# Kernel tuning notes

Measured on AMD Instinct MI355X. Metric: run time of the kernel, lower is better.

The kernel has to match this reference:

```python
import jax, jax.numpy as jnp
import numpy as np

B, L, D, T = 32, 1024, 1024, 10  # batch, seq_len, d_model, num_tags


def setup_inputs() -> dict:
    key = jax.random.key(0)
    ks = jax.random.split(key, 6)
    embeddings = jax.random.normal(ks[0], (B, L, D), jnp.float32)
    attention_mask = jnp.ones((B, L), jnp.int32)  # torchcrf requires mask[:,0]==1
    labels = jax.random.randint(ks[1], (B, L), 0, T)
    conv_w = jax.random.normal(ks[2], (T, D, 3), jnp.float32) * 0.02  # [out,in,k] torch layout
    conv_b = jnp.zeros((T,), jnp.float32)
    start_transitions = jax.random.uniform(ks[3], (T,), jnp.float32, -0.1, 0.1)
    end_transitions = jax.random.uniform(ks[4], (T,), jnp.float32, -0.1, 0.1)
    transitions = jax.random.uniform(ks[5], (T, T), jnp.float32, -0.1, 0.1)
    return dict(embeddings=embeddings, attention_mask=attention_mask, labels=labels,
                conv_w=conv_w, conv_b=conv_b, start_transitions=start_transitions,
                end_transitions=end_transitions, transitions=transitions)


def _crf_nll(emissions, labels, mask_bool, start_transitions, end_transitions, transitions):
    # emissions [B,L,T], labels [B,L] int, mask_bool [B,L]
    b, l, t = emissions.shape
    maskf = mask_bool.astype(emissions.dtype)
    # ---- numerator: score of the given tag path ----
    em_tag = jnp.take_along_axis(emissions, labels[..., None], axis=-1)[..., 0]  # [B,L]
    trans_sc = transitions[labels[:, :-1], labels[:, 1:]]                         # [B,L-1]
    num = start_transitions[labels[:, 0]] + em_tag[:, 0]
    num = num + ((trans_sc + em_tag[:, 1:]) * maskf[:, 1:]).sum(-1)
    seq_len = maskf.sum(-1).astype(jnp.int32)                                     # [B]
    last_tags = labels[jnp.arange(b), seq_len - 1]
    num = num + end_transitions[last_tags]
    # ---- denominator: forward algorithm (log partition), lax.scan over time ----
    alpha0 = start_transitions + emissions[:, 0]                                  # [B,T]

    def step(alpha, xs):
        em_t, m_t = xs  # [B,T], [B]
        nxt = jax.nn.logsumexp(alpha[:, :, None] + transitions[None] + em_t[:, None, :], axis=1)
        return jnp.where(m_t[:, None], nxt, alpha), None

    alpha, _ = jax.lax.scan(step, alpha0,
                            (emissions[:, 1:].transpose(1, 0, 2), mask_bool[:, 1:].T))
    denom = jax.nn.logsumexp(alpha + end_transitions, axis=1)                     # [B]
    return -(num - denom).sum()  # torchcrf reduction='sum', model negates


def reference(embeddings, attention_mask, labels, conv_w, conv_b,
              start_transitions, end_transitions, transitions):
    # Conv1d(d_model -> num_tags, k=3, padding='same') on [B,D,L]
    x = embeddings.transpose(0, 2, 1)  # [B,D,L]
    em = jax.lax.conv_general_dilated(x, conv_w, (1,), 'SAME',
                                      dimension_numbers=('NCH', 'OIH', 'NCH'))
    em = em.transpose(0, 2, 1) + conv_b  # [B,L,T]
    mask_bool = attention_mask.astype(bool)
    return _crf_nll(em, labels, mask_bool, start_transitions, end_transitions, transitions)
```

## Files before the change

kernel.cpp:

```cpp
#include <hip/hip_runtime.h>


#define LNEG -1e30f

static constexpr int B = 32, L = 1024, D = 1024;
static constexpr int CS = 64;
static constexpr int NC = 16;

static constexpr size_t EMPAD_OFF    = 0;
static constexpr size_t CHUNKP_OFF   = (size_t)B * L * 16;
static constexpr size_t CHUNKOFF_OFF = CHUNKP_OFF + (size_t)B * NC * 100;
static constexpr size_t WB_OFF       = CHUNKOFF_OFF + (size_t)B * NC * 12;

typedef __attribute__((ext_vector_type(8))) short short8;
typedef __attribute__((ext_vector_type(4))) short short4v;
typedef __attribute__((ext_vector_type(4))) float v4f;

static __device__ inline short f2bf(float f) {
    unsigned u = __float_as_uint(f);
    unsigned r = (u + 0x7FFFu + ((u >> 16) & 1u)) >> 16;
    return (short)r;
}

__global__ __launch_bounds__(256) void init_kernel(
    const float* __restrict__ w, const float* __restrict__ bias,
    float* __restrict__ emPad, short* __restrict__ WB, float* __restrict__ out)
{
    const int gid    = blockIdx.x * 256 + threadIdx.x;
    const int stride = gridDim.x * 256;

    for (int i = gid; i < B * L * 16; i += stride) {
        const int t = i & 15;
        emPad[i] = (t < 10) ? bias[t] : LNEG;
    }
    for (int i = gid; i < 49152; i += stride) {
        const int k8 = i >> 7;
        const int r  = i & 127;
        const int t  = r >> 3;
        const int j  = r & 7;
        const int k  = (k8 << 3) | j;
        const int kk = k >> 10;
        const int d  = k & 1023;
        WB[i] = (t < 10) ? f2bf(w[t * (D * 3) + d * 3 + kk]) : (short)0;
    }
    if (gid == 0) out[0] = 0.f;
}

static constexpr int SROW = 136;
static constexpr int LDSN = 18 * SROW;

__global__ __launch_bounds__(64) void conv_mfma_kernel(
    const float* __restrict__ emb, const short* __restrict__ WB,
    float* __restrict__ emPad)
{
    __shared__ short lds[2 * LDSN];

    const int lane = threadIdx.x;
    const unsigned bid = blockIdx.x;
    const int dh   = bid & 1;
    const int l0   = ((bid >> 1) & 63) << 4;
    const int b    = bid >> 7;
    const int g    = lane >> 4;
    const int m    = lane & 15;

    const float* embB = emb + (size_t)b * (L * D);

    v4f acc0 = {0.f, 0.f, 0.f, 0.f};
    v4f acc1 = {0.f, 0.f, 0.f, 0.f};
    v4f acc2 = {0.f, 0.f, 0.f, 0.f};

    float4 pre[9];

#define PREF(DC) do {                                                         \
    const int d0_ = (DC) * 128;                                               \
    _Pragma("unroll")                                                         \
    for (int it = 0; it < 9; ++it) {                                          \
        const int idx = lane + it * 64;                                       \
        const int r_ = idx >> 5, c4 = idx & 31;                               \
        const int gl = l0 + r_ - 1;                                           \
        float4 v = make_float4(0.f, 0.f, 0.f, 0.f);                           \
        if ((unsigned)gl < (unsigned)L)                                       \
            v = *(const float4*)(embB + (size_t)gl * D + d0_ + c4 * 4);       \
        pre[it] = v;                                                          \
    } } while (0)

#define COMMIT(BUF) do {                                                      \
    short* base_ = lds + (BUF) * LDSN;                                        \
    _Pragma("unroll")                                                         \
    for (int it = 0; it < 9; ++it) {                                          \
        const int idx = lane + it * 64;                                       \
        const int r_ = idx >> 5, c4 = idx & 31;                               \
        short4v s;                                                            \
        s.x = f2bf(pre[it].x); s.y = f2bf(pre[it].y);                         \
        s.z = f2bf(pre[it].z); s.w = f2bf(pre[it].w);                         \
        *(short4v*)(base_ + r_ * SROW + c4 * 4) = s;                          \
    } } while (0)

    const int dcBase = dh * 4;
    PREF(dcBase);
    COMMIT(0);
    __syncthreads();

    for (int q = 0; q < 4; ++q) {
        const int dc = dcBase + q;
        if (q < 3) PREF(dc + 1);

        const short* bufp = lds + (q & 1) * LDSN;
#pragma unroll
        for (int kk = 0; kk < 3; ++kk) {
            const short* arow = bufp + (m + kk) * SROW + g * 8;
            const short* wp   = WB + ((size_t)(kk * 128 + dc * 16 + g)) * 128 + m * 8;
#pragma unroll
            for (int ds = 0; ds < 4; ++ds) {
                const short8 a  = *(const short8*)(arow + ds * 32);
                const short8 bf = *(const short8*)(wp + (size_t)ds * 4 * 128);
                if (kk == 0)      acc0 = __builtin_amdgcn_mfma_f32_16x16x32_bf16(a, bf, acc0, 0, 0, 0);
                else if (kk == 1) acc1 = __builtin_amdgcn_mfma_f32_16x16x32_bf16(a, bf, acc1, 0, 0, 0);
                else              acc2 = __builtin_amdgcn_mfma_f32_16x16x32_bf16(a, bf, acc2, 0, 0, 0);
            }
        }

        if (q < 3) COMMIT((q + 1) & 1);
        __syncthreads();
    }
#undef PREF
#undef COMMIT

    if (m < 10) {
#pragma unroll
        for (int r = 0; r < 4; ++r) {
            const int row = g * 4 + r;
            const int pos = l0 + row;
            atomicAdd(&emPad[((size_t)(b * L + pos) << 4) + m],
                      acc0[r] + acc1[r] + acc2[r]);
        }
    }
}

__global__ __launch_bounds__(64) void crf_chunk_kernel(
    const float* __restrict__ emPad, const float* __restrict__ trans,
    const float* __restrict__ startT, const float* __restrict__ endT,
    const int* __restrict__ labels,
    float* __restrict__ chunkP, float* __restrict__ chunkOff,
    float* __restrict__ out)
{
    const int lane = threadIdx.x & 63;
    const int grp  = lane >> 4;
    const int i    = lane & 15;
    const int id   = blockIdx.x * 4 + grp;
    const int b    = id >> 4;
    const int c    = id & 15;

    float E[10][10];
#pragma unroll
    for (int k = 0; k < 10; ++k)
#pragma unroll
        for (int j = 0; j < 10; ++j)
            E[k][j] = __expf(trans[k * 10 + j]);

    float P[10];
#pragma unroll
    for (int j = 0; j < 10; ++j) P[j] = (i == j) ? 1.f : 0.f;
    float off = 0.f;

    const int l0 = 1 + c * CS;
    const int n  = min(CS, L - l0);
    const float* embp = emPad + ((size_t)(b * L + l0) << 4);

    float4 nx0 = *(const float4*)(embp);
    float4 nx1 = *(const float4*)(embp + 4);
    float2 nx2 = *(const float2*)(embp + 8);

    for (int s = 0; s < n; ++s) {
        const float4 e0 = nx0;
        const float4 e1 = nx1;
        const float2 e2 = nx2;
        if (s + 1 < n) {
            const float* p = embp + ((size_t)(s + 1) << 4);
            nx0 = *(const float4*)(p);
            nx1 = *(const float4*)(p + 4);
            nx2 = *(const float2*)(p + 8);
        }
        float sj[10];
        sj[0] = __expf(e0.x); sj[1] = __expf(e0.y); sj[2] = __expf(e0.z); sj[3] = __expf(e0.w);
        sj[4] = __expf(e1.x); sj[5] = __expf(e1.y); sj[6] = __expf(e1.z); sj[7] = __expf(e1.w);
        sj[8] = __expf(e2.x); sj[9] = __expf(e2.y);

        float C[10];
#pragma unroll
        for (int j = 0; j < 10; ++j) C[j] = P[0] * E[0][j];
#pragma unroll
        for (int k = 1; k < 10; ++k)
#pragma unroll
            for (int j = 0; j < 10; ++j)
                C[j] = fmaf(P[k], E[k][j], C[j]);
#pragma unroll
        for (int j = 0; j < 10; ++j) C[j] *= sj[j];

        float r = C[0];
#pragma unroll
        for (int j = 1; j < 10; ++j) r = fmaxf(r, C[j]);
        r = fmaxf(r, 1e-30f);
        const float inv = 1.f / r;
        off += __logf(r);
#pragma unroll
        for (int j = 0; j < 10; ++j) P[j] = C[j] * inv;
    }

    if (i < 10) {
        float* op = chunkP + (size_t)id * 100 + i * 10;
#pragma unroll
        for (int j = 0; j < 10; ++j) op[j] = P[j];
        chunkOff[id * 12 + i] = off;
    }

    const int* lab = labels + b * L;
    float part = 0.f;
#pragma unroll
    for (int q = 0; q < 4; ++q) {
        const int o = q * 16 + i;
        if (o < n) {
            const int pos = l0 + o;
            const int y  = lab[pos];
            const int yp = lab[pos - 1];
            part += emPad[((size_t)(b * L + pos) << 4) + y] + trans[yp * 10 + y];
            if (pos == L - 1) part += endT[y];
        }
    }
    if (c == 0 && i == 0) {
        const int y0 = lab[0];
        part += startT[y0] + emPad[((size_t)(b * L) << 4) + y0];
    }
#pragma unroll
    for (int sft = 8; sft >= 1; sft >>= 1) part += __shfl_xor(part, sft);
    if (i == 0) atomicAdd(out, -part);
}

__global__ __launch_bounds__(64) void crf_final_kernel(
    const float* __restrict__ emPad, const float* __restrict__ chunkP,
    const float* __restrict__ chunkOff, const float* __restrict__ startT,
    const float* __restrict__ endT, float* __restrict__ out)
{
    const int b = threadIdx.x;
    if (b >= B) return;

    float PA[10];
    float offA;
    {
        const float* e0 = emPad + ((size_t)(b * L) << 4);
        float A[10];
#pragma unroll
        for (int j = 0; j < 10; ++j) A[j] = startT[j] + e0[j];
        float m0 = A[0];
#pragma unroll
        for (int j = 1; j < 10; ++j) m0 = fmaxf(m0, A[j]);
#pragma unroll
        for (int j = 0; j < 10; ++j) PA[j] = __expf(A[j] - m0);
        offA = m0;
    }

    for (int c = 0; c < NC; ++c) {
        const int id = b * NC + c;
        const float* mp = chunkP + (size_t)id * 100;
        const float* op = chunkOff + id * 12;

        float mat[100];
#pragma unroll
        for (int q = 0; q < 25; ++q)
            *(float4*)&mat[q * 4] = *(const float4*)(mp + q * 4);
        float off[10];
#pragma unroll
        for (int k = 0; k < 10; ++k) off[k] = op[k];

        float mB = off[0];
#pragma unroll
        for (int k = 1; k < 10; ++k) mB = fmaxf(mB, off[k]);
        float gk[10];
#pragma unroll
        for (int k = 0; k < 10; ++k) gk[k] = PA[k] * __expf(off[k] - mB);

        float C[10];
#pragma unroll
        for (int j = 0; j < 10; ++j) C[j] = gk[0] * mat[j];
#pragma unroll
        for (int k = 1; k < 10; ++k)
#pragma unroll
            for (int j = 0; j < 10; ++j)
                C[j] = fmaf(gk[k], mat[k * 10 + j], C[j]);

        float r = C[0];
#pragma unroll
        for (int j = 1; j < 10; ++j) r = fmaxf(r, C[j]);
        r = fmaxf(r, 1e-30f);
        const float inv = 1.f / r;
        offA += mB + __logf(r);
#pragma unroll
        for (int j = 0; j < 10; ++j) PA[j] = C[j] * inv;
    }

    float s = 0.f;
#pragma unroll
    for (int j = 0; j < 10; ++j) s += PA[j] * __expf(endT[j]);
    atomicAdd(out, offA + __logf(s));
}

extern "C" void kernel_launch(void* const* d_in, const int* in_sizes, int n_in,
                              void* d_out, int out_size, void* d_ws, size_t ws_size,
                              hipStream_t stream)
{
    const float* emb    = (const float*)d_in[0];
    const int*   labels = (const int*)d_in[2];
    const float* conv_w = (const float*)d_in[3];
    const float* conv_b = (const float*)d_in[4];
    const float* startT = (const float*)d_in[5];
    const float* endT   = (const float*)d_in[6];
    const float* trans  = (const float*)d_in[7];

    float* ws       = (float*)d_ws;
    float* emPad    = ws + EMPAD_OFF;
    float* chunkP   = ws + CHUNKP_OFF;
    float* chunkOff = ws + CHUNKOFF_OFF;
    short* WB       = (short*)(ws + WB_OFF);
    float* outp     = (float*)d_out;

    hipLaunchKernelGGL(init_kernel, dim3(256), dim3(256), 0, stream,
                       conv_w, conv_b, emPad, WB, outp);
    hipLaunchKernelGGL(conv_mfma_kernel, dim3(B * 64 * 2), dim3(64), 0, stream,
                       emb, WB, emPad);
    hipLaunchKernelGGL(crf_chunk_kernel, dim3(B * NC / 4), dim3(64), 0, stream,
                       emPad, trans, startT, endT, labels, chunkP, chunkOff, outp);
    hipLaunchKernelGGL(crf_final_kernel, dim3(1), dim3(64), 0, stream,
                       emPad, chunkP, chunkOff, startT, endT, outp);
}
```

Measured before the change: 262.0 us.

## Split conv output into two buffers, drop init pass and halve CRF chunk length

The conv kernel now writes each d-half's partial emissions directly into one of two separate buffers instead of atomically adding into a bias-initialised padded buffer. This removes the large emission init loop in init_kernel and the atomic read-modify-writes. The CRF chunk kernel sums the two partials on load and uses 32 chunks of 32 steps instead of 16 of 64, doubling parallelism and shortening the sequential recurrence. The cost is extra reads in the CRF kernels and a longer serial chunk combine in the final kernel. The bf16 conversion in the LDS commit also switches to a packed intrinsic.

```diff
diff --git a/kernel.cpp b/kernel.cpp
--- a/kernel.cpp
+++ b/kernel.cpp
@@ -1,19 +1,20 @@
 #include <hip/hip_runtime.h>
+#include <hip/hip_bf16.h>
 
 
 #define LNEG -1e30f
 
 static constexpr int B = 32, L = 1024, D = 1024;
-static constexpr int CS = 64;
-static constexpr int NC = 16;
-
-static constexpr size_t EMPAD_OFF    = 0;
-static constexpr size_t CHUNKP_OFF   = (size_t)B * L * 16;
+static constexpr int CS = 32;
+static constexpr int NC = 32;
+
+static constexpr size_t EMA_OFF      = 0;
+static constexpr size_t EMB_OFF      = (size_t)B * L * 16;
+static constexpr size_t CHUNKP_OFF   = EMB_OFF + (size_t)B * L * 16;
 static constexpr size_t CHUNKOFF_OFF = CHUNKP_OFF + (size_t)B * NC * 100;
 static constexpr size_t WB_OFF       = CHUNKOFF_OFF + (size_t)B * NC * 12;
 
 typedef __attribute__((ext_vector_type(8))) short short8;
-typedef __attribute__((ext_vector_type(4))) short short4v;
 typedef __attribute__((ext_vector_type(4))) float v4f;
 
 static __device__ inline short f2bf(float f) {
@@ -22,17 +23,18 @@
     return (short)r;
 }
 
+static __device__ inline unsigned pkbf(float x, float y) {
+    __hip_bfloat162 h = __float22bfloat162_rn(make_float2(x, y));
+    unsigned u;
+    __builtin_memcpy(&u, &h, 4);
+    return u;
+}
+
 __global__ __launch_bounds__(256) void init_kernel(
-    const float* __restrict__ w, const float* __restrict__ bias,
-    float* __restrict__ emPad, short* __restrict__ WB, float* __restrict__ out)
+    const float* __restrict__ w, short* __restrict__ WB, float* __restrict__ out)
 {
     const int gid    = blockIdx.x * 256 + threadIdx.x;
     const int stride = gridDim.x * 256;
-
-    for (int i = gid; i < B * L * 16; i += stride) {
-        const int t = i & 15;
-        emPad[i] = (t < 10) ? bias[t] : LNEG;
-    }
     for (int i = gid; i < 49152; i += stride) {
         const int k8 = i >> 7;
         const int r  = i & 127;
@@ -51,7 +53,8 @@
 
 __global__ __launch_bounds__(64) void conv_mfma_kernel(
     const float* __restrict__ emb, const short* __restrict__ WB,
-    float* __restrict__ emPad)
+    const float* __restrict__ bias,
+    float* __restrict__ emA, float* __restrict__ emBp)
 {
     __shared__ short lds[2 * LDSN];
 
@@ -90,10 +93,10 @@
     for (int it = 0; it < 9; ++it) {                                          \
         const int idx = lane + it * 64;                                       \
         const int r_ = idx >> 5, c4 = idx & 31;                               \
-        short4v s;                                                            \
-        s.x = f2bf(pre[it].x); s.y = f2bf(pre[it].y);                         \
-        s.z = f2bf(pre[it].z); s.w = f2bf(pre[it].w);                         \
-        *(short4v*)(base_ + r_ * SROW + c4 * 4) = s;                          \
+        uint2 s;                                                              \
+        s.x = pkbf(pre[it].x, pre[it].y);                                     \
+        s.y = pkbf(pre[it].z, pre[it].w);                                     \
+        *(uint2*)(base_ + r_ * SROW + c4 * 4) = s;                            \
     } } while (0)
 
     const int dcBase = dh * 4;
@@ -127,18 +130,21 @@
 #undef COMMIT
 
     if (m < 10) {
+        float* dst = dh ? emBp : emA;
+        const float bt = dh ? 0.f : bias[m];
 #pragma unroll
         for (int r = 0; r < 4; ++r) {
             const int row = g * 4 + r;
             const int pos = l0 + row;
-            atomicAdd(&emPad[((size_t)(b * L + pos) << 4) + m],
-                      acc0[r] + acc1[r] + acc2[r]);
+            dst[((size_t)(b * L + pos) << 4) + m] =
+                acc0[r] + acc1[r] + acc2[r] + bt;
         }
     }
 }
 
 __global__ __launch_bounds__(64) void crf_chunk_kernel(
-    const float* __restrict__ emPad, const float* __restrict__ trans,
+    const float* __restrict__ emA, const float* __restrict__ emBp,
+    const float* __restrict__ trans,
     const float* __restrict__ startT, const float* __restrict__ endT,
     const int* __restrict__ labels,
     float* __restrict__ chunkP, float* __restrict__ chunkOff,
@@ -148,8 +154,8 @@
     const int grp  = lane >> 4;
     const int i    = lane & 15;
     const int id   = blockIdx.x * 4 + grp;
-    const int b    = id >> 4;
-    const int c    = id & 15;
+    const int b    = id >> 5;
+    const int c    = id & 31;
 
     float E[10][10];
 #pragma unroll
@@ -165,26 +171,35 @@
 
     const int l0 = 1 + c * CS;
     const int n  = min(CS, L - l0);
-    const float* embp = emPad + ((size_t)(b * L + l0) << 4);
-
-    float4 nx0 = *(const float4*)(embp);
-    float4 nx1 = *(const float4*)(embp + 4);
-    float2 nx2 = *(const float2*)(embp + 8);
+    const float* pa = emA  + ((size_t)(b * L + l0) << 4);
+    const float* pb = emBp + ((size_t)(b * L + l0) << 4);
+
+    float4 na0 = *(const float4*)(pa);
+    float4 na1 = *(const float4*)(pa + 4);
+    float2 na2 = *(const float2*)(pa + 8);
+    float4 nb0 = *(const float4*)(pb);
+    float4 nb1 = *(const float4*)(pb + 4);
+    float2 nb2 = *(const float2*)(pb + 8);
 
     for (int s = 0; s < n; ++s) {
-        const float4 e0 = nx0;
-        const float4 e1 = nx1;
-        const float2 e2 = nx2;
+        const float4 a0 = na0, a1 = na1; const float2 a2 = na2;
+        const float4 b0 = nb0, b1 = nb1; const float2 b2 = nb2;
         if (s + 1 < n) {
-            const float* p = embp + ((size_t)(s + 1) << 4);
-            nx0 = *(const float4*)(p);
-            nx1 = *(const float4*)(p + 4);
-            nx2 = *(const float2*)(p + 8);
+            const float* qa = pa + ((size_t)(s + 1) << 4);
+            const float* qb = pb + ((size_t)(s + 1) << 4);
+            na0 = *(const float4*)(qa);
+            na1 = *(const float4*)(qa + 4);
+            na2 = *(const float2*)(qa + 8);
+            nb0 = *(const float4*)(qb);
+            nb1 = *(const float4*)(qb + 4);
+            nb2 = *(const float2*)(qb + 8);
         }
         float sj[10];
-        sj[0] = __expf(e0.x); sj[1] = __expf(e0.y); sj[2] = __expf(e0.z); sj[3] = __expf(e0.w);
-        sj[4] = __expf(e1.x); sj[5] = __expf(e1.y); sj[6] = __expf(e1.z); sj[7] = __expf(e1.w);
-        sj[8] = __expf(e2.x); sj[9] = __expf(e2.y);
+        sj[0] = __expf(a0.x + b0.x); sj[1] = __expf(a0.y + b0.y);
+        sj[2] = __expf(a0.z + b0.z); sj[3] = __expf(a0.w + b0.w);
+        sj[4] = __expf(a1.x + b1.x); sj[5] = __expf(a1.y + b1.y);
+        sj[6] = __expf(a1.z + b1.z); sj[7] = __expf(a1.w + b1.w);
+        sj[8] = __expf(a2.x + b2.x); sj[9] = __expf(a2.y + b2.y);
 
         float C[10];
 #pragma unroll
@@ -217,19 +232,21 @@
     const int* lab = labels + b * L;
     float part = 0.f;
 #pragma unroll
-    for (int q = 0; q < 4; ++q) {
+    for (int q = 0; q < 2; ++q) {
         const int o = q * 16 + i;
         if (o < n) {
             const int pos = l0 + o;
             const int y  = lab[pos];
             const int yp = lab[pos - 1];
-            part += emPad[((size_t)(b * L + pos) << 4) + y] + trans[yp * 10 + y];
+            const size_t ro = (size_t)(b * L + pos) << 4;
+            part += emA[ro + y] + emBp[ro + y] + trans[yp * 10 + y];
             if (pos == L - 1) part += endT[y];
         }
     }
     if (c == 0 && i == 0) {
         const int y0 = lab[0];
-        part += startT[y0] + emPad[((size_t)(b * L) << 4) + y0];
+        const size_t r0 = (size_t)(b * L) << 4;
+        part += startT[y0] + emA[r0 + y0] + emBp[r0 + y0];
     }
 #pragma unroll
     for (int sft = 8; sft >= 1; sft >>= 1) part += __shfl_xor(part, sft);
@@ -237,9 +254,10 @@
 }
 
 __global__ __launch_bounds__(64) void crf_final_kernel(
-    const float* __restrict__ emPad, const float* __restrict__ chunkP,
-    const float* __restrict__ chunkOff, const float* __restrict__ startT,
-    const float* __restrict__ endT, float* __restrict__ out)
+    const float* __restrict__ emA, const float* __restrict__ emBp,
+    const float* __restrict__ chunkP, const float* __restrict__ chunkOff,
+    const float* __restrict__ startT, const float* __restrict__ endT,
+    float* __restrict__ out)
 {
     const int b = threadIdx.x;
     if (b >= B) return;
@@ -247,10 +265,11 @@
     float PA[10];
     float offA;
     {
-        const float* e0 = emPad + ((size_t)(b * L) << 4);
+        const float* ea = emA  + ((size_t)(b * L) << 4);
+        const float* eb = emBp + ((size_t)(b * L) << 4);
         float A[10];
 #pragma unroll
-        for (int j = 0; j < 10; ++j) A[j] = startT[j] + e0[j];
+        for (int j = 0; j < 10; ++j) A[j] = startT[j] + ea[j] + eb[j];
         float m0 = A[0];
 #pragma unroll
         for (int j = 1; j < 10; ++j) m0 = fmaxf(m0, A[j]);
@@ -317,18 +336,19 @@
     const float* trans  = (const float*)d_in[7];
 
     float* ws       = (float*)d_ws;
-    float* emPad    = ws + EMPAD_OFF;
+    float* emA      = ws + EMA_OFF;
+    float* emBp     = ws + EMB_OFF;
     float* chunkP   = ws + CHUNKP_OFF;
     float* chunkOff = ws + CHUNKOFF_OFF;
     short* WB       = (short*)(ws + WB_OFF);
     float* outp     = (float*)d_out;
 
-    hipLaunchKernelGGL(init_kernel, dim3(256), dim3(256), 0, stream,
-                       conv_w, conv_b, emPad, WB, outp);
+    hipLaunchKernelGGL(init_kernel, dim3(64), dim3(256), 0, stream,
+                       conv_w, WB, outp);
     hipLaunchKernelGGL(conv_mfma_kernel, dim3(B * 64 * 2), dim3(64), 0, stream,
-                       emb, WB, emPad);
+                       emb, WB, conv_b, emA, emBp);
     hipLaunchKernelGGL(crf_chunk_kernel, dim3(B * NC / 4), dim3(64), 0, stream,
-                       emPad, trans, startT, endT, labels, chunkP, chunkOff, outp);
+                       emA, emBp, trans, startT, endT, labels, chunkP, chunkOff, outp);
     hipLaunchKernelGGL(crf_final_kernel, dim3(1), dim3(64), 0, stream,
-                       emPad, chunkP, chunkOff, startT, endT, outp);
-}
+                       emA, emBp, chunkP, chunkOff, startT, endT, outp);
+}
```

Result: slower. 279.0 us (+6.5%).
